# Kernel tuning notes

Measured on AMD Instinct MI355X. Metric: run time of the kernel, lower is better.

Reference implementation:

```python
import jax, jax.numpy as jnp
import numpy as np

H = 768    # bert hidden size
P = 64     # num dialogue pairs
L = 2 * P  # interleaved (user,system) sequence length
C = 2      # num_classes (CRF tags)
LAM = 0.1  # lambda_mle


def setup_inputs():
    key = jax.random.key(0)
    ks = jax.random.split(key, 21)
    def rn(k, shape, s=0.05):
        return jax.random.normal(k, shape, dtype=jnp.float32) * s
    G = 4 * H
    return {
        "user_repr": rn(ks[0], (P, H), 1.0),
        "system_repr": rn(ks[1], (P, H), 1.0),
        "post_Wih0": rn(ks[2], (2, G, H)), "post_Whh0": rn(ks[3], (2, G, H)), "post_b0": rn(ks[4], (2, G)),
        "post_Wih1": rn(ks[5], (2, G, 2 * H)), "post_Whh1": rn(ks[6], (2, G, H)), "post_b1": rn(ks[7], (2, G)),
        "prior_Wih0": rn(ks[8], (2, G, H)), "prior_Whh0": rn(ks[9], (2, G, H)), "prior_b0": rn(ks[10], (2, G)),
        "prior_Wih1": rn(ks[11], (2, G, 2 * H)), "prior_Whh1": rn(ks[12], (2, G, H)), "prior_b1": rn(ks[13], (2, G)),
        "post_proj_W": rn(ks[14], (C, 2 * H)), "post_proj_b": rn(ks[15], (C,)),
        "prior_proj_W": rn(ks[16], (C, 2 * H)), "prior_proj_b": rn(ks[17], (C,)),
        "transitions": rn(ks[18], (C, C), 0.1),
        "user_I_label": jax.random.randint(ks[19], (1, P), 0, C),
        "system_I_label": jax.random.randint(ks[20], (1, P), 0, C),
    }


def _lstm_dir(x, mask, Wih, Whh, b, reverse):
    # x: [P, L, Din]; mask: [P, L] bool (True = valid step). Masked steps freeze state,
    # so each row computes the LSTM over its own prefix exactly as the per-pair loop does.
    Pn, Ln, _ = x.shape
    Hn = Whh.shape[1]
    xw = jnp.einsum('pld,gd->plg', x, Wih) + b  # [P, L, 4H] input projections (torch gate order i,f,g,o)
    def step(carry, inp):
        h, c = carry
        xw_t, m_t = inp
        gates = xw_t + h @ Whh.T
        i, f, g, o = jnp.split(gates, 4, axis=-1)
        c2 = jax.nn.sigmoid(f) * c + jax.nn.sigmoid(i) * jnp.tanh(g)
        h2 = jax.nn.sigmoid(o) * jnp.tanh(c2)
        m = m_t[:, None]
        h = jnp.where(m, h2, h)
        c = jnp.where(m, c2, c)
        return (h, c), h
    init = (jnp.zeros((Pn, Hn), x.dtype), jnp.zeros((Pn, Hn), x.dtype))
    _, hs = jax.lax.scan(step, init, (jnp.swapaxes(xw, 0, 1), mask.T), reverse=reverse)
    return jnp.swapaxes(hs, 0, 1)  # [P, L, H]


def _bilstm(x, mask, layers):
    for Wih, Whh, b in layers:
        fwd = _lstm_dir(x, mask, Wih[0], Whh[0], b[0], False)
        bwd = _lstm_dir(x, mask, Wih[1], Whh[1], b[1], True)
        x = jnp.concatenate([fwd, bwd], axis=-1)
    return x


def _forward(user_repr, system_repr,
             post_Wih0, post_Whh0, post_b0, post_Wih1, post_Whh1, post_b1,
             prior_Wih0, prior_Whh0, prior_b0, prior_Wih1, prior_Whh1, prior_b1,
             post_proj_W, post_proj_b, prior_proj_W, prior_proj_b, transitions, labs):
    seq = jnp.stack([user_repr, system_repr], axis=1).reshape(L, H)  # interleaved u0,s0,u1,s1,...
    l = 2 * (jnp.arange(P) + 1)                 # prefix length per pair
    t = jnp.arange(L)
    mask = t[None, :] < l[:, None]              # [P, L]
    xb = jnp.broadcast_to(seq[None], (P, L, H))
    # posterior branch: biLSTM over each prefix, then emissions
    post_out = _bilstm(xb, mask, [(post_Wih0, post_Whh0, post_b0), (post_Wih1, post_Whh1, post_b1)])
    em = post_out @ post_proj_W.T + post_proj_b  # [P, L, C]
    mf = mask.astype(em.dtype)
    # CRF gold score per pair
    e_lab = jnp.take_along_axis(em, jnp.broadcast_to(labs[None, :, None], (P, L, 1)), axis=2)[..., 0]
    trans_step = transitions[labs[:-1], labs[1:]]  # [L-1]
    gold = (e_lab * mf).sum(1) + (trans_step[None, :] * mf[:, 1:]).sum(1)
    # CRF forward algorithm (log partition), masked scan over time
    def fstep(alpha, inp):
        em_t, m_t = inp  # [P, C], [P]
        new = jax.nn.logsumexp(alpha[:, :, None] + transitions[None, :, :] + em_t[:, None, :], axis=1)
        return jnp.where(m_t[:, None], new, alpha), None
    alpha, _ = jax.lax.scan(fstep, em[:, 0, :], (jnp.swapaxes(em[:, 1:, :], 0, 1), mask[:, 1:].T))
    total = jax.nn.logsumexp(alpha, axis=1)
    loss_crf = jnp.mean(total - gold)
    # prior branch: prefix minus last token, take last valid hidden
    mask_p = t[None, :] < (l - 1)[:, None]
    prior_out = _bilstm(xb, mask_p, [(prior_Wih0, prior_Whh0, prior_b0), (prior_Wih1, prior_Whh1, prior_b1)])
    prior_last = jnp.take_along_axis(prior_out, jnp.broadcast_to((l - 2)[:, None, None], (P, 1, 2 * H)), axis=1)[:, 0, :]
    prior_emis = prior_last @ prior_proj_W.T + prior_proj_b  # [P, C]
    post_last = jnp.take_along_axis(em, jnp.broadcast_to((l - 1)[:, None, None], (P, 1, C)), axis=1)[:, 0, :]
    loss_mle = jnp.mean((prior_emis - jax.lax.stop_gradient(post_last)) ** 2)
    return loss_crf, loss_mle, loss_crf + LAM * loss_mle


def reference(user_repr, system_repr,
              post_Wih0, post_Whh0, post_b0, post_Wih1, post_Whh1, post_b1,
              prior_Wih0, prior_Whh0, prior_b0, prior_Wih1, prior_Whh1, prior_b1,
              post_proj_W, post_proj_b, prior_proj_W, prior_proj_b, transitions,
              user_I_label, system_I_label):
    labs = jnp.stack([user_I_label[0], system_I_label[0]], axis=1).reshape(L)
    return _forward(user_repr, system_repr,
                    post_Wih0, post_Whh0, post_b0, post_Wih1, post_Whh1, post_b1,
                    prior_Wih0, prior_Whh0, prior_b0, prior_Wih1, prior_Whh1, prior_b1,
                    post_proj_W, post_proj_b, prior_proj_W, prior_proj_b, transitions, labs)
```

## Files before the change

### kernel.cpp

```cpp
#include <hip/hip_runtime.h>


typedef short v8s __attribute__((ext_vector_type(8)));
typedef float v4f __attribute__((ext_vector_type(4)));
typedef int   v4i __attribute__((ext_vector_type(4)));
typedef unsigned short u16;

#define MFMA(a, b, c) __builtin_amdgcn_mfma_f32_16x16x32_bf16((a), (b), (c), 0, 0, 0)

static constexpr size_t WMAT    = (size_t)96 * 3072 * 8;
static constexpr size_t SLOT16  = (size_t)96 * 16 * 8;
static constexpr size_t SLOT64  = (size_t)96 * 64 * 8;
static constexpr size_t SLOT128 = (size_t)96 * 128 * 8;

static constexpr size_t OFF_EM   = 0;
static constexpr size_t SZ_EM    = (size_t)2 * 64 * 128 * 2 * 4;
static constexpr size_t OFF_XW0  = OFF_EM + SZ_EM;
static constexpr size_t SZ_XW    = (size_t)4 * 128 * 3072 * 4;
static constexpr size_t OFF_XW1  = OFF_XW0 + SZ_XW;
static constexpr size_t OFF_SEQ  = OFF_XW1 + SZ_XW;
static constexpr size_t SZ_SEQ   = SLOT128 * 2;
static constexpr size_t OFF_LABS = OFF_SEQ + SZ_SEQ;
static constexpr size_t OFF_BAR  = OFF_LABS + 512;
static constexpr size_t SZ_BAR   = 16384;
static constexpr size_t OFF_W0   = OFF_BAR + SZ_BAR;
static constexpr size_t SZ_W4    = (size_t)4 * WMAT * 2;
static constexpr size_t OFF_W1X  = OFF_W0 + SZ_W4;
static constexpr size_t OFF_W1R  = OFF_W1X + SZ_W4;
static constexpr size_t OFF_F0   = OFF_W1R + SZ_W4;
static constexpr size_t SZ_F0    = (size_t)2 * 129 * SLOT16 * 2;
static constexpr size_t OFF_H0F  = OFF_F0 + SZ_F0;
static constexpr size_t SZ_H0F   = (size_t)2 * SLOT128 * 2;
static constexpr size_t OFF_B0   = OFF_H0F + SZ_H0F;
static constexpr size_t SZ_S64   = (size_t)2 * 129 * SLOT64 * 2;
static constexpr size_t OFF_F1   = OFF_B0 + SZ_S64;
static constexpr size_t OFF_B1   = OFF_F1 + SZ_S64;
static constexpr size_t WS_NEED  = OFF_B1 + SZ_S64;

static __device__ __forceinline__ u16 f2b(float f) {
  unsigned int u = __float_as_uint(f);
  unsigned int r = (u + 0x7FFFu + ((u >> 16) & 1u)) >> 16;
  return (u16)r;
}
static __device__ __forceinline__ float b2f(u16 u) {
  return __uint_as_float(((unsigned int)u) << 16);
}
static __device__ __forceinline__ float sigf(float x) {
  return 1.0f / (1.0f + __expf(-x));
}
static __device__ __forceinline__ float tanhfast(float x) {
  return 1.0f - 2.0f / (__expf(2.0f * x) + 1.0f);
}
static __device__ __forceinline__ float lse2(float a, float b) {
  float mx = fmaxf(a, b);
  return mx + __logf(__expf(a - mx) + __expf(b - mx));
}

static __device__ __forceinline__ void gl2lds16(const void* g, void* l) {
  __builtin_amdgcn_global_load_lds((const __attribute__((address_space(1))) unsigned int*)g,
                                   (__attribute__((address_space(3))) unsigned int*)l,
                                   16, 0, 0);
}

static __device__ __forceinline__ void st2_sys(u16* p, u16 v) {
  unsigned int vv = v;
  asm volatile("global_store_short %0, %1, off sc0 sc1"
               :: "v"(p), "v"(vv) : "memory");
}
static __device__ __forceinline__ void st16_sys(u16* p, v4i v) {
  asm volatile("global_store_dwordx4 %0, %1, off sc0 sc1"
               :: "v"(p), "v"(v) : "memory");
}

static __device__ __forceinline__ void bar_signal(unsigned* base, int grp) {
  if (threadIdx.x == 0) {
    asm volatile("s_waitcnt vmcnt(0)" ::: "memory");
    unsigned o1 = __hip_atomic_fetch_add(base + grp * 32, 1u,
                                         __ATOMIC_RELAXED, __HIP_MEMORY_SCOPE_AGENT);
    if ((o1 % 6u) == 5u) {
      unsigned o2 = __hip_atomic_fetch_add(base + 256, 1u,
                                           __ATOMIC_RELAXED, __HIP_MEMORY_SCOPE_AGENT);
      if ((o2 % 8u) == 7u) {
        __hip_atomic_fetch_add(base + 288, 1u,
                               __ATOMIC_RELAXED, __HIP_MEMORY_SCOPE_AGENT);
      }
    }
  }
}
static __device__ __forceinline__ void bar_wait(unsigned* base, unsigned target) {
  if (threadIdx.x == 0) {
    int guard = 0;
    while (__hip_atomic_load(base + 288, __ATOMIC_RELAXED,
                             __HIP_MEMORY_SCOPE_AGENT) < target) {
      __builtin_amdgcn_s_sleep(1);
      if (++guard > (1 << 21)) break;
    }
  }
  __syncthreads();
}

__global__ void init_zero(u16* f0a, u16* f0b, u16* b0a, u16* b0b,
                          u16* f1a, u16* f1b, u16* b1a, u16* b1b, unsigned* bars) {
  int idx = blockIdx.x * 256 + threadIdx.x;
  if (idx < (int)SLOT16) { f0a[idx] = 0; f0b[idx] = 0; }
  b0a[idx] = 0; b0b[idx] = 0;
  f1a[idx] = 0; f1b[idx] = 0;
  b1a[idx] = 0; b1b[idx] = 0;
  if (idx < 4096) bars[idx] = 0;
}

__global__ void build_seq(const float* user, const float* sysr, const int* ulab,
                          const int* slab, u16* seqkp, int* labs) {
  int idx = blockIdx.x * 256 + threadIdx.x;
  int t = idx / 768;
  int hh = idx - t * 768;
  float v = (t & 1) ? sysr[(t >> 1) * 768 + hh] : user[(t >> 1) * 768 + hh];
  seqkp[((size_t)(hh >> 3) * 128 + t) * 8 + (hh & 7)] = f2b(v);
  if (idx < 128) labs[idx] = (idx & 1) ? slab[idx >> 1] : ulab[idx >> 1];
}

__global__ void cvt_w(const float* postWhh0, const float* priWhh0,
                      const float* postWih1, const float* priWih1,
                      const float* postWhh1, const float* priWhh1,
                      u16* W0kp, u16* W1xkp, u16* W1rkp) {
  int mat = blockIdx.y;
  int grp = mat >> 2;
  int sub = mat & 3;
  int mm = sub >> 1;
  int dirw = sub & 1;
  const float* src;
  int stride, coff;
  u16* dstb;
  if (grp == 0)      { src = mm ? priWhh0 : postWhh0; stride = 768;  coff = 0;   dstb = W0kp; }
  else if (grp == 1) { src = mm ? priWih1 : postWih1; stride = 1536; coff = 768; dstb = W1xkp; }
  else               { src = mm ? priWhh1 : postWhh1; stride = 768;  coff = 0;   dstb = W1rkp; }
  src += (size_t)dirw * 3072 * stride;
  int cid = blockIdx.x * 256 + threadIdx.x;
  int g = cid / 96;
  int kb = cid - g * 96;
  int gate = g / 768;
  int unit = g - gate * 768;
  int gp = unit * 4 + gate;
  const float* s = src + (size_t)g * stride + coff + (size_t)kb * 8;
  union { u16 h[8]; int4 v; } u;
#pragma unroll
  for (int j = 0; j < 8; ++j) u.h[j] = f2b(s[j]);
  ((int4*)(dstb + (size_t)sub * WMAT))[(size_t)kb * 3072 + gp] = u.v;
}

__global__ void __launch_bounds__(256) xw_gemm(const u16* Akp, unsigned long long Astride,
                                               const float* Wm0, const float* Wm1, int wstride,
                                               const float* bm0, const float* bm1, float* out) {
  __shared__ u16 lds[48 * 64 * 8];
  int tid = threadIdx.x;
  int lane = tid & 63;
  int wave = tid >> 6;
  int md = blockIdx.y;
  int m = md >> 1;
  int dir = md & 1;
  const u16* A = Akp + (size_t)m * Astride;
  const float* W = (m ? Wm1 : Wm0) + (size_t)dir * 3072 * wstride;
  const float* b = (m ? bm1 : bm0) + dir * 3072;
  int g0 = blockIdx.x * 64;
  int quad = lane >> 4, l15 = lane & 15;
  v4f acc[2][4];
#pragma unroll
  for (int a = 0; a < 2; ++a)
#pragma unroll
    for (int nt = 0; nt < 4; ++nt) acc[a][nt] = (v4f){0.f, 0.f, 0.f, 0.f};

  for (int hfl = 0; hfl < 2; ++hfl) {
    if (hfl) __syncthreads();
    for (int it = 0; it < 12; ++it) {
      int ck = it * 256 + tid;
      int kb = ck >> 6;
      int r = ck & 63;
      int g = g0 + r;
      const float* s = W + (size_t)g * wstride + (size_t)(hfl * 48 + kb) * 8;
      union { u16 h[8]; int4 v; } u;
#pragma unroll
      for (int j = 0; j < 8; ++j) u.h[j] = f2b(s[j]);
      *(int4*)(lds + (size_t)ck * 8) = u.v;
    }
    __syncthreads();
    for (int lt = 0; lt < 12; ++lt) {
      int kblk = (hfl * 12 + lt) * 4 + quad;
      v8s a0 = ((const v8s*)A)[(size_t)kblk * 128 + (wave * 2 + 0) * 16 + l15];
      v8s a1 = ((const v8s*)A)[(size_t)kblk * 128 + (wave * 2 + 1) * 16 + l15];
#pragma unroll
      for (int nt = 0; nt < 4; ++nt) {
        v8s bb = *(const v8s*)(lds + ((size_t)((lt * 4 + quad) * 64) + nt * 16 + l15) * 8);
        acc[0][nt] = MFMA(a0, bb, acc[0][nt]);
        acc[1][nt] = MFMA(a1, bb, acc[1][nt]);
      }
    }
  }
#pragma unroll
  for (int a = 0; a < 2; ++a)
#pragma unroll
    for (int nt = 0; nt < 4; ++nt) {
      int g = g0 + nt * 16 + l15;
      float bv = b[g];
#pragma unroll
      for (int r = 0; r < 4; ++r) {
        int trow = (wave * 2 + a) * 16 + quad * 4 + r;
        out[(size_t)(md * 128 + trow) * 3072 + g] = acc[a][nt][r] + bv;
      }
    }
}

__global__ void __launch_bounds__(256, 1) phase1_k(const u16* W0kp, const float* xw0,
                                                   u16* B0, u16* F0, u16* h0f,
                                                   unsigned* bars) {
  extern __shared__ u16 ldsraw[];
  v8s* lw = (v8s*)ldsraw;
  u16* hstg = ldsraw + 49152;
  const int tid = threadIdx.x;
  const int w = tid >> 6, lane = tid & 63, l15 = lane & 15, l4 = lane >> 4;
  const int b = blockIdx.x;
  const int chain = (b & 7) >> 1;
  const int ci = ((b >> 3) << 1) | (b & 1);
  const int grp = ci / 6;
  const int jb = ci << 4;
  const int m = chain & 1;
  const bool isf = chain >= 2;
  const int mat = m * 2 + (isf ? 0 : 1);
  unsigned* bbase = bars + chain * 512;

  {
    const v8s* Ws = (const v8s*)(W0kp) + (size_t)mat * (WMAT / 8);
    const size_t rowb = (size_t)jb * 4;
    for (int i = 0; i < 24; ++i) {
      int idx = i * 256 + tid;
      int kg = idx >> 6, r = idx & 63;
      gl2lds16(Ws + (size_t)kg * 3072 + rowb + r, (void*)(lw + (i * 256 + (w << 6))));
    }
  }
  __syncthreads();

  const int i0 = w >> 1, j0 = w & 1;
  const int u0 = i0 * 8 + l4, u1 = u0 + 4;
  const int ju0 = jb + u0, ju1 = jb + u1;
  const int p0q = j0 * 32 + l15, p1q = p0q + 16;
  float c00 = 0.f, c01 = 0.f, c10 = 0.f, c11 = 0.f;
  const bool skip = isf && (j0 == 1);
  const bool fep  = isf && (j0 == 0) && (l15 == 0);

  for (int it = 0; it < 128; ++it) {
    const int t = isf ? it : (127 - it);
    const float* xw = xw0 + (size_t)(mat * 128 + t) * 3072;
    float xi0 = xw[ju0], xf0 = xw[768 + ju0], xg0 = xw[1536 + ju0], xo0 = xw[2304 + ju0];
    float xi1 = xw[ju1], xf1 = xw[768 + ju1], xg1 = xw[1536 + ju1], xo1 = xw[2304 + ju1];
    v4f a00 = {0.f, 0.f, 0.f, 0.f}, a01 = a00, a10 = a00, a11 = a00;

    if (it) bar_wait(bbase, (unsigned)it);

    if (isf) {
      if (!skip) {
        const v8s* hs = (const v8s*)(F0 + (size_t)(m * 129 + t) * SLOT16);
#pragma unroll
        for (int kb = 0; kb < 24; ++kb) {
          int kg = kb * 4 + l4;
          v8s A0 = lw[kg * 64 + i0 * 32 + l15];
          v8s A1 = lw[kg * 64 + i0 * 32 + 16 + l15];
          v8s Bb = hs[kg * 16 + l15];
          a00 = MFMA(A0, Bb, a00);
          a10 = MFMA(A1, Bb, a10);
        }
      }
    } else {
      const v8s* hs = (const v8s*)(B0 + (size_t)(m * 129 + t + 1) * SLOT64);
#pragma unroll
      for (int kb = 0; kb < 24; ++kb) {
        int kg = kb * 4 + l4;
        v8s A0 = lw[kg * 64 + i0 * 32 + l15];
        v8s A1 = lw[kg * 64 + i0 * 32 + 16 + l15];
        v8s Bb0 = hs[kg * 64 + p0q];
        v8s Bb1 = hs[kg * 64 + p1q];
        a00 = MFMA(A0, Bb0, a00);
        a01 = MFMA(A0, Bb1, a01);
        a10 = MFMA(A1, Bb0, a10);
        a11 = MFMA(A1, Bb1, a11);
      }
    }

    if (isf) {
      if (fep) {
        float gi = sigf(a00[0] + xi0), gf = sigf(a00[1] + xf0);
        float gg = tanhfast(a00[2] + xg0), go = sigf(a00[3] + xo0);
        float cn = gf * c00 + gi * gg;
        float hn = go * tanhfast(cn);
        c00 = cn;
        u16 hb = f2b(hn);
        st2_sys(F0 + (size_t)(m * 129 + t + 1) * SLOT16 + (size_t)(ju0 >> 3) * 16 * 8 + (ju0 & 7), hb);
        h0f[(size_t)m * SLOT128 + ((size_t)(ju0 >> 3) * 128 + t) * 8 + (ju0 & 7)] = hb;
        gi = sigf(a10[0] + xi1); gf = sigf(a10[1] + xf1);
        gg = tanhfast(a10[2] + xg1); go = sigf(a10[3] + xo1);
        cn = gf * c10 + gi * gg;
        hn = go * tanhfast(cn);
        c10 = cn;
        hb = f2b(hn);
        st2_sys(F0 + (size_t)(m * 129 + t + 1) * SLOT16 + (size_t)(ju1 >> 3) * 16 * 8 + (ju1 & 7), hb);
        h0f[(size_t)m * SLOT128 + ((size_t)(ju1 >> 3) * 128 + t) * 8 + (ju1 & 7)] = hb;
      }
    } else {
      auto epi1 = [&](const v4f& ac, float& cc, int p, int loff,
                      float xi, float xf, float xg, float xo) {
        int lenp = 2 * p + 2 - m;
        bool act = t < lenp;
        float gi = sigf(ac[0] + xi), gf = sigf(ac[1] + xf);
        float gg = tanhfast(ac[2] + xg), go = sigf(ac[3] + xo);
        float cn = gf * cc + gi * gg;
        float hn = go * tanhfast(cn);
        cc = act ? cn : 0.f;
        hstg[(size_t)(i0 * 64 + p) * 8 + loff] = f2b(act ? hn : 0.f);
      };
      epi1(a00, c00, p0q, l4,     xi0, xf0, xg0, xo0);
      epi1(a01, c01, p1q, l4,     xi0, xf0, xg0, xo0);
      epi1(a10, c10, p0q, l4 + 4, xi1, xf1, xg1, xo1);
      epi1(a11, c11, p1q, l4 + 4, xi1, xf1, xg1, xo1);
    }
    __syncthreads();
    if (!isf && tid < 128) {
      v4i v = *(const v4i*)(hstg + (size_t)tid * 8);
      u16* dst = B0 + (size_t)(m * 129 + t) * SLOT64 + (size_t)(jb >> 3) * 512 + (size_t)tid * 8;
      st16_sys(dst, v);
    }
    __syncthreads();
    if (it != 127) bar_signal(bbase, grp);
  }
}

__global__ void __launch_bounds__(256, 1) phase2_k(const u16* W1x, const u16* W1r,
                                                   const float* xw1s, const u16* B0,
                                                   u16* F1, u16* B1, unsigned* bars) {
  extern __shared__ u16 ldsraw[];
  v8s* lwr = (v8s*)ldsraw;
  u16* bufb = ldsraw + 49152;
  u16* hstg = ldsraw + 73728;
  const int tid = threadIdx.x;
  const int w = tid >> 6, lane = tid & 63, l15 = lane & 15, l4 = lane >> 4;
  const int b = blockIdx.x;
  const int md = (b & 7) >> 1;
  const int ci = ((b >> 3) << 1) | (b & 1);
  const int grp = ci / 6;
  const int jb = ci << 4;
  const int m = md >> 1, dir = md & 1;
  unsigned* bbase = bars + (4 + md) * 512;
  const size_t rowb = (size_t)jb * 4;
  const v8s* Wxs = (const v8s*)(W1x) + (size_t)md * (WMAT / 8);

  {
    const v8s* Wrs = (const v8s*)(W1r) + (size_t)md * (WMAT / 8);
    for (int i = 0; i < 24; ++i) {
      int idx = i * 256 + tid;
      int kg = idx >> 6, r = idx & 63;
      gl2lds16(Wrs + (size_t)kg * 3072 + rowb + r, (void*)(lwr + (i * 256 + (w << 6))));
    }
  }

  const int i0 = w >> 1, j0 = w & 1;
  const int u0 = i0 * 8 + l4, u1 = u0 + 4;
  const int ju0 = jb + u0, ju1 = jb + u1;
  const int p0q = j0 * 32 + l15, p1q = p0q + 16;
  float c00 = 0.f, c01 = 0.f, c10 = 0.f, c11 = 0.f;
  float he00 = 0.f, he01 = 0.f, he10 = 0.f, he11 = 0.f;

  auto stage = [&](int c, int v) {
#pragma unroll
    for (int q = 0; q < 6; ++q) {
      int idx = q * 256 + tid;
      int kgl = idx >> 6, r = idx & 63;
      gl2lds16(Wxs + (size_t)(c * 24 + kgl) * 3072 + rowb + r,
               (void*)(bufb + (size_t)v * 12288 + (size_t)(q * 256 + (w << 6)) * 8));
    }
  };
  stage(0, 0);
  __syncthreads();

  for (int it = 0; it < 128; ++it) {
    const int t = dir ? (127 - it) : it;
    const v8s* hx = (const v8s*)(B0 + (size_t)(m * 129 + t) * SLOT64);
    const v8s* hr = (const v8s*)(dir ? (B1 + (size_t)(m * 129 + t + 1) * SLOT64)
                                     : (F1 + (size_t)(m * 129 + t) * SLOT64));
    const float* xw = xw1s + (size_t)(md * 128 + t) * 3072;
    float xi0 = xw[ju0], xf0 = xw[768 + ju0], xg0 = xw[1536 + ju0], xo0 = xw[2304 + ju0];
    float xi1 = xw[ju1], xf1 = xw[768 + ju1], xg1 = xw[1536 + ju1], xo1 = xw[2304 + ju1];
    v4f a00 = {0.f, 0.f, 0.f, 0.f}, a01 = a00, a10 = a00, a11 = a00;

    auto rpart = [&](int k0) {
#pragma unroll
      for (int k = 0; k < 8; ++k) {
        int kg = (k0 + k) * 4 + l4;
        v8s A0 = lwr[kg * 64 + i0 * 32 + l15];
        v8s A1 = lwr[kg * 64 + i0 * 32 + 16 + l15];
        v8s Bb0 = hr[kg * 64 + p0q];
        v8s Bb1 = hr[kg * 64 + p1q];
        a00 = MFMA(A0, Bb0, a00); a01 = MFMA(A0, Bb1, a01);
        a10 = MFMA(A1, Bb0, a10); a11 = MFMA(A1, Bb1, a11);
      }
    };
    auto xpart = [&](int c, int v) {
      const v8s* bv = (const v8s*)(bufb + (size_t)v * 12288);
#pragma unroll
      for (int k = 0; k < 6; ++k) {
        int kgl = k * 4 + l4;
        int kg = (c * 6 + k) * 4 + l4;
        v8s A0 = bv[kgl * 64 + i0 * 32 + l15];
        v8s A1 = bv[kgl * 64 + i0 * 32 + 16 + l15];
        v8s Bb0 = hx[kg * 64 + p0q];
        v8s Bb1 = hx[kg * 64 + p1q];
        a00 = MFMA(A0, Bb0, a00); a01 = MFMA(A0, Bb1, a01);
        a10 = MFMA(A1, Bb0, a10); a11 = MFMA(A1, Bb1, a11);
      }
    };

    stage(1, 1); xpart(0, 0); __syncthreads();
    stage(2, 0); xpart(1, 1); __syncthreads();
    stage(3, 1); xpart(2, 0); __syncthreads();
    xpart(3, 1);
    if (it) bar_wait(bbase, (unsigned)it);
    rpart(0); rpart(8); rpart(16);

    auto epi = [&](const v4f& ac, float& cc, float& he, int p, int loff,
                   float xi, float xf, float xg, float xo) {
      int lenp = 2 * p + 2 - m;
      bool act = t < lenp;
      float gi = sigf(ac[0] + xi), gf = sigf(ac[1] + xf);
      float gg = tanhfast(ac[2] + xg), go = sigf(ac[3] + xo);
      float cn = gf * cc + gi * gg;
      float hn = go * tanhfast(cn);
      float hv;
      if (dir) { hv = act ? hn : 0.f;  cc = act ? cn : 0.f; }
      else     { hv = act ? hn : he;   cc = act ? cn : cc;  }
      he = hv;
      hstg[(size_t)(i0 * 64 + p) * 8 + loff] = f2b(hv);
    };
    epi(a00, c00, he00, p0q, l4,     xi0, xf0, xg0, xo0);
    epi(a01, c01, he01, p1q, l4,     xi0, xf0, xg0, xo0);
    epi(a10, c10, he10, p0q, l4 + 4, xi1, xf1, xg1, xo1);
    epi(a11, c11, he11, p1q, l4 + 4, xi1, xf1, xg1, xo1);

    stage(0, 0);
    __syncthreads();
    if (tid < 128) {
      u16* hd = dir ? (B1 + (size_t)(m * 129 + t) * SLOT64)
                    : (F1 + (size_t)(m * 129 + t + 1) * SLOT64);
      v4i v = *(const v4i*)(hstg + (size_t)tid * 8);
      st16_sys(hd + (size_t)(jb >> 3) * 512 + (size_t)tid * 8, v);
    }
    __syncthreads();
    if (it != 127) bar_signal(bbase, grp);
  }
}

__global__ void __launch_bounds__(256) em_k(const u16* F1, const u16* B1,
                                            const float* pW0, const float* pb0,
                                            const float* pW1, const float* pb1, float* em) {
  int wid = blockIdx.x * 4 + (threadIdx.x >> 6);
  int lane = threadIdx.x & 63;
  int m = wid >> 13;
  int rem = wid & 8191;
  int p = rem >> 7;
  int t = rem & 127;
  const u16* hf = F1 + (size_t)(m * 129 + t + 1) * SLOT64;
  const u16* hb = B1 + (size_t)(m * 129 + t) * SLOT64;
  const float* Pw = m ? pW1 : pW0;
  const float* Pb = m ? pb1 : pb0;
  float s0 = 0.f, s1 = 0.f;
#pragma unroll
  for (int i = 0; i < 12; ++i) {
    int j = i * 64 + lane;
    size_t o = ((size_t)(j >> 3) * 64 + p) * 8 + (j & 7);
    float vf = b2f(hf[o]);
    float vb = b2f(hb[o]);
    s0 += Pw[j] * vf + Pw[768 + j] * vb;
    s1 += Pw[1536 + j] * vf + Pw[2304 + j] * vb;
  }
  for (int off = 32; off; off >>= 1) {
    s0 += __shfl_down(s0, off, 64);
    s1 += __shfl_down(s1, off, 64);
  }
  if (lane == 0) {
    em[((size_t)(m * 64 + p) * 128 + t) * 2 + 0] = s0 + Pb[0];
    em[((size_t)(m * 64 + p) * 128 + t) * 2 + 1] = s1 + Pb[1];
  }
}

__global__ void final_k(const float* em, const int* labs, const float* T, float* out) {
  int p = threadIdx.x;
  const float* emP = em + (size_t)p * 128 * 2;
  int lp = 2 * p + 2;
  float T00 = T[0], T01 = T[1], T10 = T[2], T11 = T[3];
  int prevlab = labs[0];
  float gold = emP[prevlab];
  for (int t = 1; t < lp; ++t) {
    int lb = labs[t];
    gold += emP[t * 2 + lb] + (prevlab ? (lb ? T11 : T10) : (lb ? T01 : T00));
    prevlab = lb;
  }
  float a0 = emP[0], a1 = emP[1];
  for (int t = 1; t < lp; ++t) {
    float n0 = lse2(a0 + T00, a1 + T10) + emP[t * 2];
    float n1 = lse2(a0 + T01, a1 + T11) + emP[t * 2 + 1];
    a0 = n0;
    a1 = n1;
  }
  float crf = lse2(a0, a1) - gold;
  const float* emR = em + (size_t)(64 + p) * 128 * 2;
  int lpr = 2 * p + 1;
  float d0 = emR[(lpr - 1) * 2 + 0] - emP[(lp - 1) * 2 + 0];
  float d1 = emR[(lpr - 1) * 2 + 1] - emP[(lp - 1) * 2 + 1];
  float mse = d0 * d0 + d1 * d1;
  for (int off = 32; off; off >>= 1) {
    crf += __shfl_down(crf, off, 64);
    mse += __shfl_down(mse, off, 64);
  }
  if (p == 0) {
    float lc = crf / 64.f;
    float lm = mse / 128.f;
    out[0] = lc;
    out[1] = lm;
    out[2] = lc + 0.1f * lm;
  }
}

extern "C" void kernel_launch(void* const* d_in, const int* in_sizes, int n_in,
                              void* d_out, int out_size, void* d_ws, size_t ws_size,
                              hipStream_t stream) {
  (void)in_sizes; (void)n_in; (void)out_size;
  if (ws_size < WS_NEED) return;

  const float* user     = (const float*)d_in[0];
  const float* sysr     = (const float*)d_in[1];
  const float* postWih0 = (const float*)d_in[2];
  const float* postWhh0 = (const float*)d_in[3];
  const float* postb0   = (const float*)d_in[4];
  const float* postWih1 = (const float*)d_in[5];
  const float* postWhh1 = (const float*)d_in[6];
  const float* postb1   = (const float*)d_in[7];
  const float* priWih0  = (const float*)d_in[8];
  const float* priWhh0  = (const float*)d_in[9];
  const float* prib0    = (const float*)d_in[10];
  const float* priWih1  = (const float*)d_in[11];
  const float* priWhh1  = (const float*)d_in[12];
  const float* prib1    = (const float*)d_in[13];
  const float* postPW   = (const float*)d_in[14];
  const float* postPb   = (const float*)d_in[15];
  const float* priPW    = (const float*)d_in[16];
  const float* priPb    = (const float*)d_in[17];
  const float* trans    = (const float*)d_in[18];
  const int*   ulab     = (const int*)d_in[19];
  const int*   slab     = (const int*)d_in[20];
  float* out = (float*)d_out;

  char* wsb = (char*)d_ws;
  float* em    = (float*)(wsb + OFF_EM);
  float* xw0   = (float*)(wsb + OFF_XW0);
  float* xw1s  = (float*)(wsb + OFF_XW1);
  u16* seqkp   = (u16*)(wsb + OFF_SEQ);
  int* labs    = (int*)(wsb + OFF_LABS);
  unsigned* bars = (unsigned*)(wsb + OFF_BAR);
  u16* W0kp    = (u16*)(wsb + OFF_W0);
  u16* W1xkp   = (u16*)(wsb + OFF_W1X);
  u16* W1rkp   = (u16*)(wsb + OFF_W1R);
  u16* F0      = (u16*)(wsb + OFF_F0);
  u16* h0f     = (u16*)(wsb + OFF_H0F);
  u16* B0      = (u16*)(wsb + OFF_B0);
  u16* F1      = (u16*)(wsb + OFF_F1);
  u16* B1      = (u16*)(wsb + OFF_B1);

  static bool attr_done = false;
  if (!attr_done) {
    (void)hipFuncSetAttribute(reinterpret_cast<const void*>(phase1_k),
                              hipFuncAttributeMaxDynamicSharedMemorySize, 100352);
    (void)hipFuncSetAttribute(reinterpret_cast<const void*>(phase2_k),
                              hipFuncAttributeMaxDynamicSharedMemorySize, 149504);
    attr_done = true;
  }

  init_zero<<<192, 256, 0, stream>>>(
      F0, F0 + (size_t)129 * SLOT16,
      B0 + (size_t)128 * SLOT64, B0 + (size_t)(129 + 128) * SLOT64,
      F1, F1 + (size_t)129 * SLOT64,
      B1 + (size_t)128 * SLOT64, B1 + (size_t)(129 + 128) * SLOT64, bars);

  build_seq<<<384, 256, 0, stream>>>(user, sysr, ulab, slab, seqkp, labs);

  cvt_w<<<dim3(1152, 12), 256, 0, stream>>>(postWhh0, priWhh0, postWih1, priWih1,
                                            postWhh1, priWhh1, W0kp, W1xkp, W1rkp);

  xw_gemm<<<dim3(48, 4), 256, 0, stream>>>(seqkp, 0ULL, postWih0, priWih0, 768,
                                           postb0, prib0, xw0);

  phase1_k<<<192, 256, 100352, stream>>>(W0kp, xw0, B0, F0, h0f, bars);

  xw_gemm<<<dim3(48, 4), 256, 0, stream>>>(h0f, (unsigned long long)SLOT128,
                                           postWih1, priWih1, 1536, postb1, prib1, xw1s);

  phase2_k<<<192, 256, 149504, stream>>>(W1xkp, W1rkp, xw1s, B0, F1, B1, bars);

  em_k<<<4096, 256, 0, stream>>>(F1, B1, postPW, postPb, priPW, priPb, em);

  final_k<<<1, 64, 0, stream>>>(em, labs, trans, out);
}
```

Before: 3.682 ms.

## Flatten grid barrier with replicated release flags; read layer-1 input weights directly from global

The hierarchical two-level atomic barrier becomes a single counter. The last arriver writes the generation number to eight replicated flag lines, and each group polls its own line with a longer sleep. In phase 2, the double-buffered LDS staging of the input-side weight chunks is removed. Those weights are now read straight from global/L2 inside the MFMA loop, which frees LDS and removes intra-step __syncthreads. The trade-off is contention from 48 atomics on one counter and global-load latency in the x-part GEMM, which is no longer hidden by the staging pipeline.

```diff
diff --git a/kernel.cpp b/kernel.cpp
--- a/kernel.cpp
+++ b/kernel.cpp
@@ -71,29 +71,32 @@
   asm volatile("global_store_dwordx4 %0, %1, off sc0 sc1"
                :: "v"(p), "v"(v) : "memory");
 }
-
-static __device__ __forceinline__ void bar_signal(unsigned* base, int grp) {
+static __device__ __forceinline__ void st4_sys(unsigned* p, unsigned v) {
+  asm volatile("global_store_dword %0, %1, off sc0 sc1"
+               :: "v"(p), "v"(v) : "memory");
+}
+
+static __device__ __forceinline__ void bar_signal(unsigned* base) {
   if (threadIdx.x == 0) {
     asm volatile("s_waitcnt vmcnt(0)" ::: "memory");
-    unsigned o1 = __hip_atomic_fetch_add(base + grp * 32, 1u,
-                                         __ATOMIC_RELAXED, __HIP_MEMORY_SCOPE_AGENT);
-    if ((o1 % 6u) == 5u) {
-      unsigned o2 = __hip_atomic_fetch_add(base + 256, 1u,
-                                           __ATOMIC_RELAXED, __HIP_MEMORY_SCOPE_AGENT);
-      if ((o2 % 8u) == 7u) {
-        __hip_atomic_fetch_add(base + 288, 1u,
-                               __ATOMIC_RELAXED, __HIP_MEMORY_SCOPE_AGENT);
-      }
-    }
-  }
-}
-static __device__ __forceinline__ void bar_wait(unsigned* base, unsigned target) {
+    unsigned old = __hip_atomic_fetch_add(base, 1u,
+                                          __ATOMIC_RELAXED, __HIP_MEMORY_SCOPE_AGENT);
+    if ((old % 48u) == 47u) {
+      unsigned g = old / 48u + 1u;
+#pragma unroll
+      for (int r = 0; r < 8; ++r) st4_sys(base + 64 + r * 32, g);
+      asm volatile("s_waitcnt vmcnt(0)" ::: "memory");
+    }
+  }
+}
+static __device__ __forceinline__ void bar_wait(unsigned* base, int grp, unsigned target) {
   if (threadIdx.x == 0) {
+    unsigned* rep = base + 64 + grp * 32;
     int guard = 0;
-    while (__hip_atomic_load(base + 288, __ATOMIC_RELAXED,
+    while (__hip_atomic_load(rep, __ATOMIC_RELAXED,
                              __HIP_MEMORY_SCOPE_AGENT) < target) {
-      __builtin_amdgcn_s_sleep(1);
-      if (++guard > (1 << 21)) break;
+      __builtin_amdgcn_s_sleep(4);
+      if (++guard > (1 << 20)) break;
     }
   }
   __syncthreads();
@@ -253,7 +256,7 @@
     float xi1 = xw[ju1], xf1 = xw[768 + ju1], xg1 = xw[1536 + ju1], xo1 = xw[2304 + ju1];
     v4f a00 = {0.f, 0.f, 0.f, 0.f}, a01 = a00, a10 = a00, a11 = a00;
 
-    if (it) bar_wait(bbase, (unsigned)it);
+    if (it) bar_wait(bbase, grp, (unsigned)it);
 
     if (isf) {
       if (!skip) {
@@ -327,7 +330,7 @@
       st16_sys(dst, v);
     }
     __syncthreads();
-    if (it != 127) bar_signal(bbase, grp);
+    if (it != 127) bar_signal(bbase);
   }
 }
 
@@ -336,8 +339,7 @@
                                                    u16* F1, u16* B1, unsigned* bars) {
   extern __shared__ u16 ldsraw[];
   v8s* lwr = (v8s*)ldsraw;
-  u16* bufb = ldsraw + 49152;
-  u16* hstg = ldsraw + 73728;
+  u16* hstg = ldsraw + 49152;
   const int tid = threadIdx.x;
   const int w = tid >> 6, lane = tid & 63, l15 = lane & 15, l4 = lane >> 4;
   const int b = blockIdx.x;
@@ -358,6 +360,7 @@
       gl2lds16(Wrs + (size_t)kg * 3072 + rowb + r, (void*)(lwr + (i * 256 + (w << 6))));
     }
   }
+  __syncthreads();
 
   const int i0 = w >> 1, j0 = w & 1;
   const int u0 = i0 * 8 + l4, u1 = u0 + 4;
@@ -365,18 +368,6 @@
   const int p0q = j0 * 32 + l15, p1q = p0q + 16;
   float c00 = 0.f, c01 = 0.f, c10 = 0.f, c11 = 0.f;
   float he00 = 0.f, he01 = 0.f, he10 = 0.f, he11 = 0.f;
-
-  auto stage = [&](int c, int v) {
-#pragma unroll
-    for (int q = 0; q < 6; ++q) {
-      int idx = q * 256 + tid;
-      int kgl = idx >> 6, r = idx & 63;
-      gl2lds16(Wxs + (size_t)(c * 24 + kgl) * 3072 + rowb + r,
-               (void*)(bufb + (size_t)v * 12288 + (size_t)(q * 256 + (w << 6)) * 8));
-    }
-  };
-  stage(0, 0);
-  __syncthreads();
 
   for (int it = 0; it < 128; ++it) {
     const int t = dir ? (127 - it) : it;
@@ -388,39 +379,29 @@
     float xi1 = xw[ju1], xf1 = xw[768 + ju1], xg1 = xw[1536 + ju1], xo1 = xw[2304 + ju1];
     v4f a00 = {0.f, 0.f, 0.f, 0.f}, a01 = a00, a10 = a00, a11 = a00;
 
-    auto rpart = [&](int k0) {
-#pragma unroll
-      for (int k = 0; k < 8; ++k) {
-        int kg = (k0 + k) * 4 + l4;
-        v8s A0 = lwr[kg * 64 + i0 * 32 + l15];
-        v8s A1 = lwr[kg * 64 + i0 * 32 + 16 + l15];
-        v8s Bb0 = hr[kg * 64 + p0q];
-        v8s Bb1 = hr[kg * 64 + p1q];
-        a00 = MFMA(A0, Bb0, a00); a01 = MFMA(A0, Bb1, a01);
-        a10 = MFMA(A1, Bb0, a10); a11 = MFMA(A1, Bb1, a11);
-      }
-    };
-    auto xpart = [&](int c, int v) {
-      const v8s* bv = (const v8s*)(bufb + (size_t)v * 12288);
-#pragma unroll
-      for (int k = 0; k < 6; ++k) {
-        int kgl = k * 4 + l4;
-        int kg = (c * 6 + k) * 4 + l4;
-        v8s A0 = bv[kgl * 64 + i0 * 32 + l15];
-        v8s A1 = bv[kgl * 64 + i0 * 32 + 16 + l15];
-        v8s Bb0 = hx[kg * 64 + p0q];
-        v8s Bb1 = hx[kg * 64 + p1q];
-        a00 = MFMA(A0, Bb0, a00); a01 = MFMA(A0, Bb1, a01);
-        a10 = MFMA(A1, Bb0, a10); a11 = MFMA(A1, Bb1, a11);
-      }
-    };
-
-    stage(1, 1); xpart(0, 0); __syncthreads();
-    stage(2, 0); xpart(1, 1); __syncthreads();
-    stage(3, 1); xpart(2, 0); __syncthreads();
-    xpart(3, 1);
-    if (it) bar_wait(bbase, (unsigned)it);
-    rpart(0); rpart(8); rpart(16);
+#pragma unroll 4
+    for (int kb = 0; kb < 24; ++kb) {
+      int kg = kb * 4 + l4;
+      v8s A0 = Wxs[(size_t)kg * 3072 + rowb + i0 * 32 + l15];
+      v8s A1 = Wxs[(size_t)kg * 3072 + rowb + i0 * 32 + 16 + l15];
+      v8s Bb0 = hx[kg * 64 + p0q];
+      v8s Bb1 = hx[kg * 64 + p1q];
+      a00 = MFMA(A0, Bb0, a00); a01 = MFMA(A0, Bb1, a01);
+      a10 = MFMA(A1, Bb0, a10); a11 = MFMA(A1, Bb1, a11);
+    }
+
+    if (it) bar_wait(bbase, grp, (unsigned)it);
+
+#pragma unroll 4
+    for (int kb = 0; kb < 24; ++kb) {
+      int kg = kb * 4 + l4;
+      v8s A0 = lwr[kg * 64 + i0 * 32 + l15];
+      v8s A1 = lwr[kg * 64 + i0 * 32 + 16 + l15];
+      v8s Bb0 = hr[kg * 64 + p0q];
+      v8s Bb1 = hr[kg * 64 + p1q];
+      a00 = MFMA(A0, Bb0, a00); a01 = MFMA(A0, Bb1, a01);
+      a10 = MFMA(A1, Bb0, a10); a11 = MFMA(A1, Bb1, a11);
+    }
 
     auto epi = [&](const v4f& ac, float& cc, float& he, int p, int loff,
                    float xi, float xf, float xg, float xo) {
@@ -441,7 +422,6 @@
     epi(a10, c10, he10, p0q, l4 + 4, xi1, xf1, xg1, xo1);
     epi(a11, c11, he11, p1q, l4 + 4, xi1, xf1, xg1, xo1);
 
-    stage(0, 0);
     __syncthreads();
     if (tid < 128) {
       u16* hd = dir ? (B1 + (size_t)(m * 129 + t) * SLOT64)
@@ -450,7 +430,7 @@
       st16_sys(hd + (size_t)(jb >> 3) * 512 + (size_t)tid * 8, v);
     }
     __syncthreads();
-    if (it != 127) bar_signal(bbase, grp);
+    if (it != 127) bar_signal(bbase);
   }
 }
 
@@ -575,7 +555,7 @@
     (void)hipFuncSetAttribute(reinterpret_cast<const void*>(phase1_k),
                               hipFuncAttributeMaxDynamicSharedMemorySize, 100352);
     (void)hipFuncSetAttribute(reinterpret_cast<const void*>(phase2_k),
-                              hipFuncAttributeMaxDynamicSharedMemorySize, 149504);
+                              hipFuncAttributeMaxDynamicSharedMemorySize, 100352);
     attr_done = true;
   }
 
@@ -598,7 +578,7 @@
   xw_gemm<<<dim3(48, 4), 256, 0, stream>>>(h0f, (unsigned long long)SLOT128,
                                            postWih1, priWih1, 1536, postb1, prib1, xw1s);
 
-  phase2_k<<<192, 256, 149504, stream>>>(W1xkp, W1rkp, xw1s, B0, F1, B1, bars);
+  phase2_k<<<192, 256, 100352, stream>>>(W1xkp, W1rkp, xw1s, B0, F1, B1, bars);
 
   em_k<<<4096, 256, 0, stream>>>(F1, B1, postPW, postPb, priPW, priPb, em);
 
```

New measurement: 3.723 ms. No clear change (+1.1%).
